# Performance work log

Measured on AMD Instinct MI355X. Metric: run time of the kernel, lower is better.

The kernel has to match this reference:

```python
import jax, jax.numpy as jnp
import numpy as np


def setup_inputs() -> dict:
    key = jax.random.key(0)
    k1, k2 = jax.random.split(key)
    z = jax.random.normal(k1, (16, 256, 32, 32), dtype=jnp.float32)
    emb = jax.random.normal(k2, (8192, 256), dtype=jnp.float32)
    return {"z": z, "emb": emb}


def reference(z, emb):
    B, C, H, W = z.shape
    # [B,C,H,W] -> [B*H*W, C], distances in fp32 for precision
    z_f = jnp.transpose(z, (0, 2, 3, 1)).reshape(-1, C).astype(jnp.float32)
    e = emb.astype(jnp.float32)
    # squared-distance expansion: ||z||^2 - 2 z.e + ||e||^2  -> [N, K]
    d = (
        jnp.sum(z_f * z_f, axis=1, keepdims=True)
        - 2.0 * (z_f @ e.T)
        + jnp.sum(e * e, axis=1)[None, :]
    )
    idx = jnp.argmin(d, axis=1)  # [N]
    out = emb[idx].astype(z.dtype)  # codebook gather
    return jnp.transpose(out.reshape(B, H, W, C), (0, 3, 1, 2))
```

## Files before the change

### kernel.cpp

```cpp
#include <hip/hip_runtime.h>
#include <stdint.h>

#define NB   16
#define CD   256
#define HW   1024
#define NQ   16384
#define KCN  8192

typedef unsigned long long u64;
typedef unsigned short     u16;
using f32x4  = __attribute__((ext_vector_type(4))) float;
using bf16x8 = __attribute__((ext_vector_type(8))) __bf16;

#define ZTB_OFF  0
#define EMBB_OFF 8388608
#define EH_OFF   12582912
#define CAND_OFF 12615680

static __device__ __forceinline__ void gl_lds16(const void* g, void* l) {
  __builtin_amdgcn_global_load_lds(
      (const __attribute__((address_space(1))) void*)g,
      (__attribute__((address_space(3))) void*)l, 16, 0, 0);
}

static __device__ __forceinline__ unsigned bf16r(float x) {
  unsigned u = __float_as_uint(x);
  return (u + 0x7fffu + ((u >> 16) & 1u)) >> 16;
}

static __device__ __forceinline__ u64 umin64(u64 a, u64 b) { return a < b ? a : b; }
static __device__ __forceinline__ u64 umax64(u64 a, u64 b) { return a < b ? b : a; }

__global__ __launch_bounds__(256) void k_prep(const float* __restrict__ z,
                                              const float* __restrict__ emb,
                                              u16* __restrict__ zTb,
                                              u16* __restrict__ embB,
                                              float* __restrict__ eH) {
  const int bx = (int)blockIdx.x;
  if (bx < 1024) {
    __shared__ float tile[64][65];
    const int b   = bx >> 6;
    const int hwT = (bx >> 2) & 15;
    const int cT  = bx & 3;
    const int tx  = threadIdx.x & 63;
    const int ty  = threadIdx.x >> 6;
    const float* src = z + (size_t)(b * CD + cT * 64) * HW + hwT * 64;
#pragma unroll
    for (int i = 0; i < 16; ++i) {
      const int c_l = ty + 4 * i;
      tile[c_l][tx] = src[(size_t)c_l * HW + tx];
    }
    __syncthreads();
    const size_t dbase = (size_t)(b * HW + hwT * 64) * CD + cT * 64;
#pragma unroll
    for (int i = 0; i < 16; ++i) {
      const int hw_l = ty + 4 * i;
      zTb[dbase + (size_t)hw_l * CD + tx] = (u16)bf16r(tile[tx][hw_l]);
    }
  } else {
    const int wave = (bx - 1024) * 4 + ((int)threadIdx.x >> 6);
    const int lane = threadIdx.x & 63;
#pragma unroll
    for (int it = 0; it < 8; ++it) {
      const int row = wave * 8 + it;
      const float4 v = *(const float4*)(emb + (size_t)row * CD + lane * 4);
      uint2 pk;
      pk.x = bf16r(v.x) | (bf16r(v.y) << 16);
      pk.y = bf16r(v.z) | (bf16r(v.w) << 16);
      *(uint2*)(embB + (size_t)row * CD + lane * 4) = pk;
      float s = v.x * v.x + v.y * v.y + v.z * v.z + v.w * v.w;
#pragma unroll
      for (int off = 32; off; off >>= 1) s += __shfl_xor(s, off, 64);
      if (lane == 0) eH[row] = 0.5f * s + 1024.0f;
    }
  }
}


#define WAITV(N) asm volatile("s_waitcnt vmcnt(" #N ")" ::: "memory")
#define MEMFENCE() asm volatile("" ::: "memory")

__global__ __launch_bounds__(256, 2) void k_argmin(const u16* __restrict__ zTb,
                                                   const u16* __restrict__ embB,
                                                   const float* __restrict__ eH,
                                                   u64* __restrict__ cand) {
  __shared__ __align__(16) u16 Bs[4][128 * 64];

  const int tid  = (int)threadIdx.x;
  const int w    = tid >> 6;
  const int lane = tid & 63;
  const int l15  = lane & 15, quad = lane >> 4;
  const int q0    = (int)(blockIdx.x >> 3) * 128;
  const int split = (int)(blockIdx.x & 7);

  bf16x8 Af[2][4][2];
  {
    const char* aB = (const char*)zTb
                   + ((size_t)(q0 + w * 32 + l15) * CD + quad * 8) * 2;
#pragma unroll
    for (int i = 0; i < 2; ++i)
#pragma unroll
      for (int kc = 0; kc < 4; ++kc)
#pragma unroll
        for (int ks = 0; ks < 2; ++ks)
          Af[i][kc][ks] = *(const bf16x8*)(aB + i * 8192 + kc * 128 + ks * 64);
  }
  MEMFENCE();

  const char* bS = (const char*)embB + (size_t)split * (1024 * 512)
                 + (size_t)(w * 32 + (lane >> 3)) * 512
                 + (size_t)(((lane & 7) ^ (lane >> 3)) * 16);
  const int ldsW = w * 4096 + lane * 16;

#define STAGE(RING, NT_, KC_)                                                  \
  do {                                                                         \
    const char* _s = bS + (NT_) * 65536 + (KC_) * 128;                         \
    char* _d = (char*)Bs[RING] + ldsW;                                         \
    gl_lds16(_s,         _d);                                                  \
    gl_lds16(_s + 4096,  _d + 1024);                                           \
    gl_lds16(_s + 8192,  _d + 2048);                                           \
    gl_lds16(_s + 12288, _d + 3072);                                           \
  } while (0)

  const int bR0 = l15 * 128 + ((quad ^ (l15 & 7)) * 16);
  const int bR1 = bR0 ^ 64;

  f32x4 acc[2][8];
  float b1[8][2], b2[8][2];
  const float FMAX = __uint_as_float(0x7F7FFFFFu);
#pragma unroll
  for (int s = 0; s < 8; ++s) { b1[s][0] = b1[s][1] = FMAX; b2[s][0] = b2[s][1] = FMAX; }

  STAGE(0, 0, 0); MEMFENCE();
  STAGE(1, 0, 1); MEMFENCE();
  STAGE(2, 0, 2); MEMFENCE();

#define MFMA_INT(RING, KC_)                                                    \
  do {                                                                         \
    const char* _b = (const char*)Bs[RING];                                    \
    _Pragma("unroll")                                                          \
    for (int ks = 0; ks < 2; ++ks) {                                           \
      bf16x8 bfr[8];                                                           \
      const int _o = ks ? bR1 : bR0;                                           \
      _Pragma("unroll")                                                        \
      for (int j = 0; j < 8; ++j)                                              \
        bfr[j] = *(const bf16x8*)(_b + j * 2048 + _o);                         \
      __builtin_amdgcn_s_setprio(1);                                           \
      _Pragma("unroll")                                                        \
      for (int i = 0; i < 2; ++i)                                              \
        _Pragma("unroll")                                                      \
        for (int j = 0; j < 8; ++j)                                            \
          acc[i][j] = __builtin_amdgcn_mfma_f32_16x16x32_bf16(                 \
              Af[i][KC_][ks], bfr[j], acc[i][j], 0, 0, 0);                     \
      __builtin_amdgcn_s_setprio(0);                                           \
    }                                                                          \
  } while (0)

#define EPILOGUE(NT_)                                                          \
  do {                                                                         \
    _Pragma("unroll")                                                          \
    for (int i = 0; i < 2; ++i)                                                \
      _Pragma("unroll")                                                        \
      for (int r = 0; r < 4; ++r) {                                            \
        const int s = i * 4 + r;                                               \
        float kq[8];                                                           \
        _Pragma("unroll")                                                      \
        for (int j = 0; j < 8; ++j)                                            \
          kq[j] = __uint_as_float(                                             \
              (__float_as_uint(eh[j] - acc[i][j][r]) & ~63u)                   \
              | (unsigned)((NT_) * 8 + j));                                    \
        _Pragma("unroll")                                                      \
        for (int h = 0; h < 2; ++h) {                                          \
          const float k0 = kq[4 * h], k1 = kq[4 * h + 1];                      \
          const float k2 = kq[4 * h + 2], k3 = kq[4 * h + 3];                  \
          const float lo01 = fminf(k0, k1), hi01 = fmaxf(k0, k1);              \
          const float lo23 = fminf(k2, k3), hi23 = fmaxf(k2, k3);              \
          const float best = fminf(lo01, lo23);                                \
          const float sec  = fminf(fmaxf(lo01, lo23), fminf(hi01, hi23));      \
          b2[s][h] = fminf(fmaxf(best, b1[s][h]), fminf(sec, b2[s][h]));       \
          b1[s][h] = fminf(best, b1[s][h]);                                    \
        }                                                                      \
      }                                                                        \
  } while (0)

  float eh[8];

  for (int nt = 0; nt < 7; ++nt) {
    const int n0 = split * 1024 + nt * 128;
#pragma unroll
    for (int i = 0; i < 2; ++i)
#pragma unroll
      for (int j = 0; j < 8; ++j) acc[i][j] = f32x4{0.f, 0.f, 0.f, 0.f};

    WAITV(8); __builtin_amdgcn_s_barrier(); MEMFENCE();
    STAGE(3, nt, 3); MEMFENCE();
#pragma unroll
    for (int j = 0; j < 8; ++j) eh[j] = eH[n0 + j * 16 + l15];
    MEMFENCE();
    MFMA_INT(0, 0);
    WAITV(16); __builtin_amdgcn_s_barrier(); MEMFENCE();
    STAGE(0, nt + 1, 0); MEMFENCE();
    MFMA_INT(1, 1);
    WAITV(16); __builtin_amdgcn_s_barrier(); MEMFENCE();
    STAGE(1, nt + 1, 1); MEMFENCE();
    MFMA_INT(2, 2);
    WAITV(16); __builtin_amdgcn_s_barrier(); MEMFENCE();
    STAGE(2, nt + 1, 2); MEMFENCE();
    MFMA_INT(3, 3);

    EPILOGUE(nt);
  }

  {
    const int n0 = split * 1024 + 7 * 128;
#pragma unroll
    for (int i = 0; i < 2; ++i)
#pragma unroll
      for (int j = 0; j < 8; ++j) acc[i][j] = f32x4{0.f, 0.f, 0.f, 0.f};

    WAITV(8); __builtin_amdgcn_s_barrier(); MEMFENCE();
    STAGE(3, 7, 3); MEMFENCE();
#pragma unroll
    for (int j = 0; j < 8; ++j) eh[j] = eH[n0 + j * 16 + l15];
    MEMFENCE();
    MFMA_INT(0, 0);

    WAITV(16); __builtin_amdgcn_s_barrier(); MEMFENCE();
    MFMA_INT(1, 1);

    WAITV(12); __builtin_amdgcn_s_barrier(); MEMFENCE();
    MFMA_INT(2, 2);

    WAITV(8); __builtin_amdgcn_s_barrier(); MEMFENCE();
    MFMA_INT(3, 3);

    EPILOGUE(7);
  }
#undef STAGE
#undef MFMA_INT
#undef EPILOGUE

#pragma unroll
  for (int s = 0; s < 8; ++s) {
#pragma unroll
    for (int h = 0; h < 2; ++h) {
      u64 x1 = ((u64)__float_as_uint(b1[s][h]) << 32) | (unsigned)l15;
      u64 x2 = ((u64)__float_as_uint(b2[s][h]) << 32) | (unsigned)l15;
#pragma unroll
      for (int off = 1; off < 16; off <<= 1) {
        const u64 o1 = __shfl_xor(x1, off, 64);
        const u64 o2 = __shfl_xor(x2, off, 64);
        const u64 lo = umin64(x1, o1);
        const u64 hi = umax64(x1, o1);
        x1 = lo;
        x2 = umin64(hi, umin64(x2, o2));
      }
      if (l15 == 0) {
        const int i = s >> 2, r = s & 3;
        const int q = q0 + w * 32 + i * 16 + quad * 4 + r;
        const unsigned kb1 = (unsigned)(x1 >> 32), kb2 = (unsigned)(x2 >> 32);
        const int n1 = split * 1024 + (int)((kb1 >> 3) & 7) * 128
                       + (int)(kb1 & 7) * 16 + (int)(x1 & 15);
        const int n2 = split * 1024 + (int)((kb2 >> 3) & 7) * 128
                       + (int)(kb2 & 7) * 16 + (int)(x2 & 15);
        cand[(size_t)q * 32 + split * 4 + h * 2 + 0] = ((u64)kb1 << 32) | (unsigned)n1;
        cand[(size_t)q * 32 + split * 4 + h * 2 + 1] = ((u64)kb2 << 32) | (unsigned)n2;
      }
    }
  }
}

__global__ __launch_bounds__(256) void k_pick_out(const float* __restrict__ z,
                                                  const float* __restrict__ emb,
                                                  const u64* __restrict__ cand,
                                                  float* __restrict__ out) {
  __shared__ float zs[16][257];
  __shared__ float tile[16][257];
  const int t    = (int)threadIdx.x;
  const int lane = t & 63;
  const int wv   = t >> 6;
  const int sub  = lane >> 4;
  const int l15  = lane & 15;
  const int q0b  = (int)blockIdx.x * 16;
  const int b    = q0b >> 10, hw0 = q0b & 1023;
  const int q    = q0b + wv * 4 + sub;
  const int hwl  = wv * 4 + sub;

  {
    const float* zp = z + ((size_t)(b * CD + t)) * HW + hw0;
    const float4 a0 = *(const float4*)(zp + 0);
    const float4 a1 = *(const float4*)(zp + 4);
    const float4 a2 = *(const float4*)(zp + 8);
    const float4 a3 = *(const float4*)(zp + 12);
    zs[0][t] = a0.x;  zs[1][t] = a0.y;  zs[2][t] = a0.z;  zs[3][t] = a0.w;
    zs[4][t] = a1.x;  zs[5][t] = a1.y;  zs[6][t] = a1.z;  zs[7][t] = a1.w;
    zs[8][t] = a2.x;  zs[9][t] = a2.y;  zs[10][t] = a2.z; zs[11][t] = a2.w;
    zs[12][t] = a3.x; zs[13][t] = a3.y; zs[14][t] = a3.z; zs[15][t] = a3.w;
  }
  __syncthreads();

  const u64* cp = cand + (size_t)q * 32 + l15 * 2;
  const u64 v0 = cp[0], v1 = cp[1];
  u64 s0 = umin64(v0, v1), s1 = umax64(v0, v1), s2 = ~0ull, s3 = ~0ull;
#pragma unroll
  for (int off = 1; off < 16; off <<= 1) {
    const u64 b0 = __shfl_xor(s0, off, 64);
    const u64 b1 = __shfl_xor(s1, off, 64);
    const u64 b2 = __shfl_xor(s2, off, 64);
    const u64 b3 = __shfl_xor(s3, off, 64);
    const u64 c0 = umin64(s0, b0);
    const u64 c1 = umin64(umin64(s1, b1), umax64(s0, b0));
    const u64 c2 = umin64(umin64(s2, b2),
                          umin64(umax64(s1, b0), umax64(s0, b1)));
    const u64 c3 = umin64(umin64(umin64(s3, b3), umax64(s2, b0)),
                          umin64(umax64(s0, b2), umax64(s1, b1)));
    s0 = c0; s1 = c1; s2 = c2; s3 = c3;
  }
  const u64 sel[4] = {s0, s1, s2, s3};

  float zq[16];
#pragma unroll
  for (int j = 0; j < 16; ++j) zq[j] = zs[hwl][j * 16 + l15];

  double bd = 1e300;
  int bi = 0x7fffffff;
  float keep[16];
#pragma unroll
  for (int j = 0; j < 16; ++j) keep[j] = 0.f;
#pragma unroll
  for (int c4 = 0; c4 < 4; ++c4) {
    const int idx = (int)(unsigned)(sel[c4] & 0xffffffffull);
    const float* er = emb + (size_t)idx * CD;
    float ev[16];
#pragma unroll
    for (int j = 0; j < 16; ++j) ev[j] = er[j * 16 + l15];
    double s = 0.0;
#pragma unroll
    for (int j = 0; j < 16; ++j) {
      const double d = (double)zq[j] - (double)ev[j];
      s += d * d;
    }
#pragma unroll
    for (int off = 1; off < 16; off <<= 1) s += __shfl_xor(s, off, 64);
    const bool better = (s < bd) || (s == bd && idx < bi);
    if (better) {
      bd = s; bi = idx;
#pragma unroll
      for (int j = 0; j < 16; ++j) keep[j] = ev[j];
    }
  }
#pragma unroll
  for (int j = 0; j < 16; ++j) tile[hwl][j * 16 + l15] = keep[j];
  __syncthreads();
  const int cluster = t >> 4;
  const int ll      = t & 15;
  float* obase = out + (size_t)b * CD * HW + hw0 + ll;
#pragma unroll
  for (int j = 0; j < 16; ++j) {
    const int c = 16 * j + cluster;
    obase[(size_t)c * HW] = tile[ll][c];
  }
}

extern "C" void kernel_launch(void* const* d_in, const int* in_sizes, int n_in,
                              void* d_out, int out_size, void* d_ws, size_t ws_size,
                              hipStream_t stream) {
  const float* z   = (const float*)d_in[0];
  const float* emb = (const float*)d_in[1];
  float* out = (float*)d_out;

  char* ws = (char*)d_ws;
  u16*   zTb  = (u16*)(ws + ZTB_OFF);
  u16*   embB = (u16*)(ws + EMBB_OFF);
  float* eH   = (float*)(ws + EH_OFF);
  u64*   cand = (u64*)(ws + CAND_OFF);

  k_prep<<<1280, 256, 0, stream>>>(z, emb, zTb, embB, eH);
  k_argmin<<<1024, 256, 0, stream>>>(zTb, embB, eH, cand);
  k_pick_out<<<1024, 256, 0, stream>>>(z, emb, cand, out);
}
```

Measured before the change: 173.3 us.

## Retile argmin GEMM into 2x2 wave grid with 64-code, 128-deep K stages

Each wave now owns a 64-query by 32-code subtile (2x2 wave arrangement) instead of 32 queries by all 128 codes. The LDS ring stages 64 codes by 128 K-elements per slot, with a new XOR swizzle. Each wave therefore issues fewer LDS B-fragment reads per MFMA, because 4 A fragments share each B load. The top-2 epilogue now tracks 16 rows with a 2-way compare, candidate encoding is changed to match, and eH loads are prefetched one tile ahead. The cost is more A-fragment registers per wave (32 bf16x8), which may pressure occupancy at 2 blocks per CU.

```diff
diff --git a/kernel.cpp b/kernel.cpp
--- a/kernel.cpp
+++ b/kernel.cpp
@@ -84,7 +84,7 @@
                                                    const u16* __restrict__ embB,
                                                    const float* __restrict__ eH,
                                                    u64* __restrict__ cand) {
-  __shared__ __align__(16) u16 Bs[4][128 * 64];
+  __shared__ __align__(16) u16 Bs[4][64 * 128];
 
   const int tid  = (int)threadIdx.x;
   const int w    = tid >> 6;
@@ -92,180 +92,186 @@
   const int l15  = lane & 15, quad = lane >> 4;
   const int q0    = (int)(blockIdx.x >> 3) * 128;
   const int split = (int)(blockIdx.x & 7);
-
-  bf16x8 Af[2][4][2];
+  const int wq0 = (w & 1) * 64;
+  const int nh  = w >> 1;
+
+  bf16x8 Af[4][2][4];
   {
-    const char* aB = (const char*)zTb
-                   + ((size_t)(q0 + w * 32 + l15) * CD + quad * 8) * 2;
-#pragma unroll
-    for (int i = 0; i < 2; ++i)
-#pragma unroll
-      for (int kc = 0; kc < 4; ++kc)
-#pragma unroll
-        for (int ks = 0; ks < 2; ++ks)
-          Af[i][kc][ks] = *(const bf16x8*)(aB + i * 8192 + kc * 128 + ks * 64);
+    const char* aB = (const char*)zTb + (size_t)(q0 + wq0 + l15) * 512 + quad * 16;
+#pragma unroll
+    for (int i = 0; i < 4; ++i)
+#pragma unroll
+      for (int kc = 0; kc < 2; ++kc)
+#pragma unroll
+        for (int ks = 0; ks < 4; ++ks)
+          Af[i][kc][ks] = *(const bf16x8*)(aB + i * 8192 + kc * 256 + ks * 64);
   }
   MEMFENCE();
 
-  const char* bS = (const char*)embB + (size_t)split * (1024 * 512)
-                 + (size_t)(w * 32 + (lane >> 3)) * 512
-                 + (size_t)(((lane & 7) ^ (lane >> 3)) * 16);
-  const int ldsW = w * 4096 + lane * 16;
-
-#define STAGE(RING, NT_, KC_)                                                  \
+  const char* bS = (const char*)embB + (size_t)split * 524288
+                 + (size_t)(tid >> 4) * 512
+                 + (size_t)(((tid & 15) ^ ((tid >> 4) & 7)) * 16);
+  const int ldsW = tid * 16;
+
+#define STAGE(RING, SRCOFF)                                                    \
   do {                                                                         \
-    const char* _s = bS + (NT_) * 65536 + (KC_) * 128;                         \
+    const char* _s = bP + (SRCOFF);                                            \
     char* _d = (char*)Bs[RING] + ldsW;                                         \
     gl_lds16(_s,         _d);                                                  \
-    gl_lds16(_s + 4096,  _d + 1024);                                           \
-    gl_lds16(_s + 8192,  _d + 2048);                                           \
-    gl_lds16(_s + 12288, _d + 3072);                                           \
+    gl_lds16(_s + 8192,  _d + 4096);                                           \
+    gl_lds16(_s + 16384, _d + 8192);                                           \
+    gl_lds16(_s + 24576, _d + 12288);                                          \
+    MEMFENCE();                                                                \
   } while (0)
 
-  const int bR0 = l15 * 128 + ((quad ^ (l15 & 7)) * 16);
-  const int bR1 = bR0 ^ 64;
-
-  f32x4 acc[2][8];
-  float b1[8][2], b2[8][2];
-  const float FMAX = __uint_as_float(0x7F7FFFFFu);
-#pragma unroll
-  for (int s = 0; s < 8; ++s) { b1[s][0] = b1[s][1] = FMAX; b2[s][0] = b2[s][1] = FMAX; }
-
-  STAGE(0, 0, 0); MEMFENCE();
-  STAGE(1, 0, 1); MEMFENCE();
-  STAGE(2, 0, 2); MEMFENCE();
-
-#define MFMA_INT(RING, KC_)                                                    \
+  const int bRow = (nh * 32 + l15) * 256;
+  const int gx   = l15 & 7;
+
+#define MFMA_INT(RING, KCH)                                                    \
   do {                                                                         \
-    const char* _b = (const char*)Bs[RING];                                    \
+    const char* _b = (const char*)Bs[RING] + bRow;                             \
+    __builtin_amdgcn_s_setprio(1);                                             \
     _Pragma("unroll")                                                          \
-    for (int ks = 0; ks < 2; ++ks) {                                           \
-      bf16x8 bfr[8];                                                           \
-      const int _o = ks ? bR1 : bR0;                                           \
+    for (int ks = 0; ks < 4; ++ks) {                                           \
+      const int _o = ((ks * 4 + quad) ^ gx) * 16;                              \
+      const bf16x8 bf0 = *(const bf16x8*)(_b + _o);                            \
+      const bf16x8 bf1 = *(const bf16x8*)(_b + 4096 + _o);                     \
       _Pragma("unroll")                                                        \
-      for (int j = 0; j < 8; ++j)                                              \
-        bfr[j] = *(const bf16x8*)(_b + j * 2048 + _o);                         \
-      __builtin_amdgcn_s_setprio(1);                                           \
+      for (int i = 0; i < 4; ++i)                                              \
+        acc[i][0] = __builtin_amdgcn_mfma_f32_16x16x32_bf16(Af[i][KCH][ks],    \
+                                                            bf0, acc[i][0],    \
+                                                            0, 0, 0);          \
       _Pragma("unroll")                                                        \
-      for (int i = 0; i < 2; ++i)                                              \
-        _Pragma("unroll")                                                      \
-        for (int j = 0; j < 8; ++j)                                            \
-          acc[i][j] = __builtin_amdgcn_mfma_f32_16x16x32_bf16(                 \
-              Af[i][KC_][ks], bfr[j], acc[i][j], 0, 0, 0);                     \
-      __builtin_amdgcn_s_setprio(0);                                           \
+      for (int i = 0; i < 4; ++i)                                              \
+        acc[i][1] = __builtin_amdgcn_mfma_f32_16x16x32_bf16(Af[i][KCH][ks],    \
+                                                            bf1, acc[i][1],    \
+                                                            0, 0, 0);          \
+    }                                                                          \
+    __builtin_amdgcn_s_setprio(0);                                             \
+  } while (0)
+
+#define ACCZERO()                                                              \
+  do {                                                                         \
+    _Pragma("unroll")                                                          \
+    for (int i = 0; i < 4; ++i) {                                              \
+      acc[i][0] = f32x4{0.f, 0.f, 0.f, 0.f};                                   \
+      acc[i][1] = f32x4{0.f, 0.f, 0.f, 0.f};                                   \
     }                                                                          \
   } while (0)
 
-#define EPILOGUE(NT_)                                                          \
+#define EPILOGUE(NC, EH0, EH1)                                                 \
   do {                                                                         \
     _Pragma("unroll")                                                          \
-    for (int i = 0; i < 2; ++i)                                                \
+    for (int i = 0; i < 4; ++i)                                                \
       _Pragma("unroll")                                                        \
       for (int r = 0; r < 4; ++r) {                                            \
         const int s = i * 4 + r;                                               \
-        float kq[8];                                                           \
-        _Pragma("unroll")                                                      \
-        for (int j = 0; j < 8; ++j)                                            \
-          kq[j] = __uint_as_float(                                             \
-              (__float_as_uint(eh[j] - acc[i][j][r]) & ~63u)                   \
-              | (unsigned)((NT_) * 8 + j));                                    \
-        _Pragma("unroll")                                                      \
-        for (int h = 0; h < 2; ++h) {                                          \
-          const float k0 = kq[4 * h], k1 = kq[4 * h + 1];                      \
-          const float k2 = kq[4 * h + 2], k3 = kq[4 * h + 3];                  \
-          const float lo01 = fminf(k0, k1), hi01 = fmaxf(k0, k1);              \
-          const float lo23 = fminf(k2, k3), hi23 = fmaxf(k2, k3);              \
-          const float best = fminf(lo01, lo23);                                \
-          const float sec  = fminf(fmaxf(lo01, lo23), fminf(hi01, hi23));      \
-          b2[s][h] = fminf(fmaxf(best, b1[s][h]), fminf(sec, b2[s][h]));       \
-          b1[s][h] = fminf(best, b1[s][h]);                                    \
-        }                                                                      \
+        const unsigned kb0 = (__float_as_uint((EH0) - acc[i][0][r]) & ~31u)    \
+                             | (unsigned)((NC) * 2 + 0);                       \
+        const unsigned kb1 = (__float_as_uint((EH1) - acc[i][1][r]) & ~31u)    \
+                             | (unsigned)((NC) * 2 + 1);                       \
+        const float k0 = __uint_as_float(kb0), k1 = __uint_as_float(kb1);      \
+        const float lo = fminf(k0, k1), hi = fmaxf(k0, k1);                    \
+        b2[s] = fminf(fmaxf(lo, b1[s]), fminf(hi, b2[s]));                     \
+        b1[s] = fminf(lo, b1[s]);                                              \
       }                                                                        \
   } while (0)
 
-  float eh[8];
-
-  for (int nt = 0; nt < 7; ++nt) {
-    const int n0 = split * 1024 + nt * 128;
-#pragma unroll
-    for (int i = 0; i < 2; ++i)
-#pragma unroll
-      for (int j = 0; j < 8; ++j) acc[i][j] = f32x4{0.f, 0.f, 0.f, 0.f};
-
-    WAITV(8); __builtin_amdgcn_s_barrier(); MEMFENCE();
-    STAGE(3, nt, 3); MEMFENCE();
-#pragma unroll
-    for (int j = 0; j < 8; ++j) eh[j] = eH[n0 + j * 16 + l15];
-    MEMFENCE();
+  f32x4 acc[4][2];
+  float b1[16], b2[16];
+  const float FMAX = __uint_as_float(0x7F7FFFFFu);
+#pragma unroll
+  for (int s = 0; s < 16; ++s) { b1[s] = FMAX; b2[s] = FMAX; }
+
+  const float* ehP = eH + split * 1024 + nh * 32 + l15;
+  float ehA[2], ehB[2], ehAn[2], ehBn[2];
+
+  const char* bP = bS;
+  STAGE(0, 0);
+  ehA[0] = ehP[0];  ehA[1] = ehP[16];  MEMFENCE();
+  STAGE(1, 256);
+  STAGE(2, 32768);
+  ehB[0] = ehP[64]; ehB[1] = ehP[80]; MEMFENCE();
+  const float* ehPn = ehP + 128;
+
+  for (int ntp = 0; ntp < 7; ++ntp) {
+    const int nca = 2 * ntp, ncb = 2 * ntp + 1;
+
+    ACCZERO();
+    WAITV(12); __builtin_amdgcn_s_barrier(); MEMFENCE();
+    STAGE(3, 33024);
     MFMA_INT(0, 0);
-    WAITV(16); __builtin_amdgcn_s_barrier(); MEMFENCE();
-    STAGE(0, nt + 1, 0); MEMFENCE();
+
+    WAITV(10); __builtin_amdgcn_s_barrier(); MEMFENCE();
+    STAGE(0, 65536);
+    ehAn[0] = ehPn[0]; ehAn[1] = ehPn[16]; MEMFENCE();
     MFMA_INT(1, 1);
-    WAITV(16); __builtin_amdgcn_s_barrier(); MEMFENCE();
-    STAGE(1, nt + 1, 1); MEMFENCE();
-    MFMA_INT(2, 2);
-    WAITV(16); __builtin_amdgcn_s_barrier(); MEMFENCE();
-    STAGE(2, nt + 1, 2); MEMFENCE();
-    MFMA_INT(3, 3);
-
-    EPILOGUE(nt);
+    EPILOGUE(nca, ehA[0], ehA[1]);
+
+    ACCZERO();
+    WAITV(12); __builtin_amdgcn_s_barrier(); MEMFENCE();
+    STAGE(1, 65792);
+    MFMA_INT(2, 0);
+
+    WAITV(10); __builtin_amdgcn_s_barrier(); MEMFENCE();
+    STAGE(2, 98304);
+    ehBn[0] = ehPn[64]; ehBn[1] = ehPn[80]; MEMFENCE();
+    MFMA_INT(3, 1);
+    EPILOGUE(ncb, ehB[0], ehB[1]);
+
+    ehA[0] = ehAn[0]; ehA[1] = ehAn[1];
+    ehB[0] = ehBn[0]; ehB[1] = ehBn[1];
+    bP += 65536;
+    ehPn += 128;
   }
 
   {
-    const int n0 = split * 1024 + 7 * 128;
-#pragma unroll
-    for (int i = 0; i < 2; ++i)
-#pragma unroll
-      for (int j = 0; j < 8; ++j) acc[i][j] = f32x4{0.f, 0.f, 0.f, 0.f};
-
-    WAITV(8); __builtin_amdgcn_s_barrier(); MEMFENCE();
-    STAGE(3, 7, 3); MEMFENCE();
-#pragma unroll
-    for (int j = 0; j < 8; ++j) eh[j] = eH[n0 + j * 16 + l15];
-    MEMFENCE();
+    ACCZERO();
+    WAITV(12); __builtin_amdgcn_s_barrier(); MEMFENCE();
+    STAGE(3, 33024);
     MFMA_INT(0, 0);
 
-    WAITV(16); __builtin_amdgcn_s_barrier(); MEMFENCE();
+    WAITV(10); __builtin_amdgcn_s_barrier(); MEMFENCE();
     MFMA_INT(1, 1);
-
-    WAITV(12); __builtin_amdgcn_s_barrier(); MEMFENCE();
-    MFMA_INT(2, 2);
-
-    WAITV(8); __builtin_amdgcn_s_barrier(); MEMFENCE();
-    MFMA_INT(3, 3);
-
-    EPILOGUE(7);
+    EPILOGUE(14, ehA[0], ehA[1]);
+
+    ACCZERO();
+    WAITV(6); __builtin_amdgcn_s_barrier(); MEMFENCE();
+    MFMA_INT(2, 0);
+
+    WAITV(0); __builtin_amdgcn_s_barrier(); MEMFENCE();
+    MFMA_INT(3, 1);
+    EPILOGUE(15, ehB[0], ehB[1]);
   }
 #undef STAGE
 #undef MFMA_INT
+#undef ACCZERO
 #undef EPILOGUE
 
 #pragma unroll
-  for (int s = 0; s < 8; ++s) {
-#pragma unroll
-    for (int h = 0; h < 2; ++h) {
-      u64 x1 = ((u64)__float_as_uint(b1[s][h]) << 32) | (unsigned)l15;
-      u64 x2 = ((u64)__float_as_uint(b2[s][h]) << 32) | (unsigned)l15;
-#pragma unroll
-      for (int off = 1; off < 16; off <<= 1) {
-        const u64 o1 = __shfl_xor(x1, off, 64);
-        const u64 o2 = __shfl_xor(x2, off, 64);
-        const u64 lo = umin64(x1, o1);
-        const u64 hi = umax64(x1, o1);
-        x1 = lo;
-        x2 = umin64(hi, umin64(x2, o2));
-      }
-      if (l15 == 0) {
-        const int i = s >> 2, r = s & 3;
-        const int q = q0 + w * 32 + i * 16 + quad * 4 + r;
-        const unsigned kb1 = (unsigned)(x1 >> 32), kb2 = (unsigned)(x2 >> 32);
-        const int n1 = split * 1024 + (int)((kb1 >> 3) & 7) * 128
-                       + (int)(kb1 & 7) * 16 + (int)(x1 & 15);
-        const int n2 = split * 1024 + (int)((kb2 >> 3) & 7) * 128
-                       + (int)(kb2 & 7) * 16 + (int)(x2 & 15);
-        cand[(size_t)q * 32 + split * 4 + h * 2 + 0] = ((u64)kb1 << 32) | (unsigned)n1;
-        cand[(size_t)q * 32 + split * 4 + h * 2 + 1] = ((u64)kb2 << 32) | (unsigned)n2;
-      }
+  for (int s = 0; s < 16; ++s) {
+    u64 x1 = ((u64)__float_as_uint(b1[s]) << 32) | (unsigned)l15;
+    u64 x2 = ((u64)__float_as_uint(b2[s]) << 32) | (unsigned)l15;
+#pragma unroll
+    for (int off = 1; off < 16; off <<= 1) {
+      const u64 o1 = __shfl_xor(x1, off, 64);
+      const u64 o2 = __shfl_xor(x2, off, 64);
+      const u64 lo = umin64(x1, o1);
+      const u64 hi = umax64(x1, o1);
+      x1 = lo;
+      x2 = umin64(hi, umin64(x2, o2));
+    }
+    if (l15 == 0) {
+      const int i = s >> 2, r = s & 3;
+      const int q = q0 + wq0 + i * 16 + quad * 4 + r;
+      const unsigned kb1 = (unsigned)(x1 >> 32), kb2 = (unsigned)(x2 >> 32);
+      const int id1 = (int)(kb1 & 31u), id2 = (int)(kb2 & 31u);
+      const int n1 = split * 1024 + (id1 >> 1) * 64 + nh * 32
+                     + (id1 & 1) * 16 + (int)(x1 & 15);
+      const int n2 = split * 1024 + (id2 >> 1) * 64 + nh * 32
+                     + (id2 & 1) * 16 + (int)(x2 & 15);
+      cand[(size_t)q * 32 + split * 4 + nh * 2 + 0] = ((u64)kb1 << 32) | (unsigned)n1;
+      cand[(size_t)q * 32 + split * 4 + nh * 2 + 1] = ((u64)kb2 << 32) | (unsigned)n2;
     }
   }
 }
```

Result: no change. 176.7 us (+2.0%).

## Widen pick_out blocks to 64 queries with XOR-swizzled LDS transpose

Applied to the files above, without the earlier changes.

The final pick/output kernel now handles 64 spatial positions per block instead of 16, with each wave doing four query groups. z is loaded and out is stored as 64-float contiguous rows per channel, giving 256-byte coalesced transactions instead of 64-byte float4 segments. An XOR swizzle on the shared tile replaces padding to avoid bank conflicts. The aim is better global-memory coalescing, at the cost of a 4x smaller grid (256 blocks) and more registers per thread.

```diff
diff --git a/kernel.cpp b/kernel.cpp
--- a/kernel.cpp
+++ b/kernel.cpp
@@ -240,6 +240,7 @@
 #undef MFMA_INT
 #undef EPILOGUE
 
+  const int wh = w >> 1;
 #pragma unroll
   for (int s = 0; s < 8; ++s) {
 #pragma unroll
@@ -274,91 +275,99 @@
                                                   const float* __restrict__ emb,
                                                   const u64* __restrict__ cand,
                                                   float* __restrict__ out) {
-  __shared__ float zs[16][257];
-  __shared__ float tile[16][257];
+  __shared__ float zs[64][256];
   const int t    = (int)threadIdx.x;
   const int lane = t & 63;
   const int wv   = t >> 6;
   const int sub  = lane >> 4;
   const int l15  = lane & 15;
-  const int q0b  = (int)blockIdx.x * 16;
+  const int q0b  = (int)blockIdx.x * 64;
   const int b    = q0b >> 10, hw0 = q0b & 1023;
-  const int q    = q0b + wv * 4 + sub;
-  const int hwl  = wv * 4 + sub;
 
   {
-    const float* zp = z + ((size_t)(b * CD + t)) * HW + hw0;
-    const float4 a0 = *(const float4*)(zp + 0);
-    const float4 a1 = *(const float4*)(zp + 4);
-    const float4 a2 = *(const float4*)(zp + 8);
-    const float4 a3 = *(const float4*)(zp + 12);
-    zs[0][t] = a0.x;  zs[1][t] = a0.y;  zs[2][t] = a0.z;  zs[3][t] = a0.w;
-    zs[4][t] = a1.x;  zs[5][t] = a1.y;  zs[6][t] = a1.z;  zs[7][t] = a1.w;
-    zs[8][t] = a2.x;  zs[9][t] = a2.y;  zs[10][t] = a2.z; zs[11][t] = a2.w;
-    zs[12][t] = a3.x; zs[13][t] = a3.y; zs[14][t] = a3.z; zs[15][t] = a3.w;
+    const float* zb = z + ((size_t)(b * CD + wv * 64)) * HW + hw0;
+    const int sw = lane & 31;
+#pragma unroll 8
+    for (int i = 0; i < 64; ++i) {
+      const float v = zb[(size_t)i * HW + lane];
+      zs[lane][(wv * 64 + i) ^ sw] = v;
+    }
   }
   __syncthreads();
 
-  const u64* cp = cand + (size_t)q * 32 + l15 * 2;
-  const u64 v0 = cp[0], v1 = cp[1];
-  u64 s0 = umin64(v0, v1), s1 = umax64(v0, v1), s2 = ~0ull, s3 = ~0ull;
-#pragma unroll
-  for (int off = 1; off < 16; off <<= 1) {
-    const u64 b0 = __shfl_xor(s0, off, 64);
-    const u64 b1 = __shfl_xor(s1, off, 64);
-    const u64 b2 = __shfl_xor(s2, off, 64);
-    const u64 b3 = __shfl_xor(s3, off, 64);
-    const u64 c0 = umin64(s0, b0);
-    const u64 c1 = umin64(umin64(s1, b1), umax64(s0, b0));
-    const u64 c2 = umin64(umin64(s2, b2),
-                          umin64(umax64(s1, b0), umax64(s0, b1)));
-    const u64 c3 = umin64(umin64(umin64(s3, b3), umax64(s2, b0)),
-                          umin64(umax64(s0, b2), umax64(s1, b1)));
-    s0 = c0; s1 = c1; s2 = c2; s3 = c3;
-  }
-  const u64 sel[4] = {s0, s1, s2, s3};
-
-  float zq[16];
-#pragma unroll
-  for (int j = 0; j < 16; ++j) zq[j] = zs[hwl][j * 16 + l15];
-
-  double bd = 1e300;
-  int bi = 0x7fffffff;
-  float keep[16];
-#pragma unroll
-  for (int j = 0; j < 16; ++j) keep[j] = 0.f;
-#pragma unroll
-  for (int c4 = 0; c4 < 4; ++c4) {
-    const int idx = (int)(unsigned)(sel[c4] & 0xffffffffull);
-    const float* er = emb + (size_t)idx * CD;
-    float ev[16];
-#pragma unroll
-    for (int j = 0; j < 16; ++j) ev[j] = er[j * 16 + l15];
-    double s = 0.0;
-#pragma unroll
-    for (int j = 0; j < 16; ++j) {
-      const double d = (double)zq[j] - (double)ev[j];
-      s += d * d;
-    }
-#pragma unroll
-    for (int off = 1; off < 16; off <<= 1) s += __shfl_xor(s, off, 64);
-    const bool better = (s < bd) || (s == bd && idx < bi);
-    if (better) {
-      bd = s; bi = idx;
-#pragma unroll
-      for (int j = 0; j < 16; ++j) keep[j] = ev[j];
-    }
-  }
-#pragma unroll
-  for (int j = 0; j < 16; ++j) tile[hwl][j * 16 + l15] = keep[j];
+  float keep[4][16];
+#pragma unroll
+  for (int it = 0; it < 4; ++it) {
+    const int hwl = wv * 16 + it * 4 + sub;
+    const int q   = q0b + hwl;
+
+    const u64* cp = cand + (size_t)q * 32 + l15 * 2;
+    const u64 v0 = cp[0], v1 = cp[1];
+    u64 s0 = umin64(v0, v1), s1 = umax64(v0, v1), s2 = ~0ull, s3 = ~0ull;
+#pragma unroll
+    for (int off = 1; off < 16; off <<= 1) {
+      const u64 b0 = __shfl_xor(s0, off, 64);
+      const u64 b1 = __shfl_xor(s1, off, 64);
+      const u64 b2 = __shfl_xor(s2, off, 64);
+      const u64 b3 = __shfl_xor(s3, off, 64);
+      const u64 c0 = umin64(s0, b0);
+      const u64 c1 = umin64(umin64(s1, b1), umax64(s0, b0));
+      const u64 c2 = umin64(umin64(s2, b2),
+                            umin64(umax64(s1, b0), umax64(s0, b1)));
+      const u64 c3 = umin64(umin64(umin64(s3, b3), umax64(s2, b0)),
+                            umin64(umax64(s0, b2), umax64(s1, b1)));
+      s0 = c0; s1 = c1; s2 = c2; s3 = c3;
+    }
+    const u64 sel[4] = {s0, s1, s2, s3};
+
+    const int swq = hwl & 31;
+    float zq[16];
+#pragma unroll
+    for (int j = 0; j < 16; ++j) zq[j] = zs[hwl][(j * 16 + l15) ^ swq];
+
+    double bd = 1e300;
+    int bi = 0x7fffffff;
+#pragma unroll
+    for (int j = 0; j < 16; ++j) keep[it][j] = 0.f;
+#pragma unroll
+    for (int c4 = 0; c4 < 4; ++c4) {
+      const int idx = (int)(unsigned)(sel[c4] & 0xffffffffull);
+      const float* er = emb + (size_t)idx * CD;
+      float ev[16];
+#pragma unroll
+      for (int j = 0; j < 16; ++j) ev[j] = er[j * 16 + l15];
+      double s = 0.0;
+#pragma unroll
+      for (int j = 0; j < 16; ++j) {
+        const double d = (double)zq[j] - (double)ev[j];
+        s += d * d;
+      }
+#pragma unroll
+      for (int off = 1; off < 16; off <<= 1) s += __shfl_xor(s, off, 64);
+      const bool better = (s < bd) || (s == bd && idx < bi);
+      if (better) {
+        bd = s; bi = idx;
+#pragma unroll
+        for (int j = 0; j < 16; ++j) keep[it][j] = ev[j];
+      }
+    }
+  }
+
   __syncthreads();
-  const int cluster = t >> 4;
-  const int ll      = t & 15;
-  float* obase = out + (size_t)b * CD * HW + hw0 + ll;
-#pragma unroll
-  for (int j = 0; j < 16; ++j) {
-    const int c = 16 * j + cluster;
-    obase[(size_t)c * HW] = tile[ll][c];
+#pragma unroll
+  for (int it = 0; it < 4; ++it) {
+    const int hwl = wv * 16 + it * 4 + sub;
+    const int swq = hwl & 31;
+#pragma unroll
+    for (int j = 0; j < 16; ++j) zs[hwl][(j * 16 + l15) ^ swq] = keep[it][j];
+  }
+  __syncthreads();
+  {
+    float* ob = out + ((size_t)(b * CD + wv * 64)) * HW + hw0;
+    const int sw = lane & 31;
+#pragma unroll 8
+    for (int i = 0; i < 64; ++i)
+      ob[(size_t)i * HW + lane] = zs[lane][(wv * 64 + i) ^ sw];
   }
 }
 
@@ -377,5 +386,5 @@
 
   k_prep<<<1280, 256, 0, stream>>>(z, emb, zTb, embB, eH);
   k_argmin<<<1024, 256, 0, stream>>>(zTb, embB, eH, cand);
-  k_pick_out<<<1024, 256, 0, stream>>>(z, emb, cand, out);
-}
+  k_pick_out<<<256, 256, 0, stream>>>(z, emb, cand, out);
+}
```

After: 182.4 us. 5.3% more time.
